# Kernel optimization log

Hardware: AMD Instinct MI355X
Metric: run time of the kernel (lower is better)

Reference implementation:

```python
import jax, jax.numpy as jnp
import numpy as np
from jax import lax

G0, G1 = 16, 16
UNITS = 256


def setup_inputs() -> dict:
    key = jax.random.key(0)
    ks = jax.random.split(key, 20)
    B, H, W, C = 64, 512, 512, 3
    U = UNITS
    flat = 12 * 12 * 3  # after two VALID 3x3 convs on 16x16x3
    inp = {
        'image': jax.random.normal(ks[0], (B, H, W, C), jnp.float32),
        'section': jax.random.uniform(ks[1], (B, 3), jnp.float32),
        'h0': jax.random.normal(ks[2], (B, U), jnp.float32) * 0.1,
        'c0': jax.random.normal(ks[3], (B, U), jnp.float32) * 0.1,
        'conv1_k': jax.random.normal(ks[4], (3, 3, C, 3), jnp.float32) * 0.2,
        'conv1_b': jnp.zeros((3,), jnp.float32),
        'conv2_k': jax.random.normal(ks[5], (3, 3, 3, 3), jnp.float32) * 0.2,
        'conv2_b': jnp.zeros((3,), jnp.float32),
        'dense_w': jax.random.normal(ks[6], (flat, U), jnp.float32) * (1.0 / np.sqrt(flat)),
        'dense_b': jnp.zeros((U,), jnp.float32),
        'lstm_k': jax.random.normal(ks[7], (U, 4 * U), jnp.float32) * (1.0 / np.sqrt(U)),
        'lstm_rk': jax.random.normal(ks[8], (U, 4 * U), jnp.float32) * (1.0 / np.sqrt(U)),
        'lstm_b': jnp.zeros((4 * U,), jnp.float32),
        'nsc_w1': jax.random.normal(ks[9], (U, U), jnp.float32) * (1.0 / np.sqrt(U)),
        'nsc_b1': jnp.zeros((U,), jnp.float32),
        'nsc_w2': jax.random.normal(ks[10], (U, 3), jnp.float32) * (1.0 / np.sqrt(U)),
        'nsc_b2': jnp.zeros((3,), jnp.float32),
    }
    return inp


def _interpolate(image, section):
    # image: (B,H,W,C); section: (B,3) = (x, y, scale); coords in [0,1],
    # mapped linearly onto grid indices with constant (clamp) extension,
    # matching tfp.math.batch_interp_regular_nd_grid over image axes 1,2.
    B, H, W, C = image.shape
    starts = section[:, :2]                       # (B,2)
    stops = section[:, :2] + section[:, 2:]       # (B,2) broadcast scale
    t0 = jnp.linspace(0.0, 1.0, G0)               # along grid_dim[0]
    alpha = jnp.linspace(0.0, 1.0, G1)            # along grid_dim[1]
    # p0[b,i,j]: coordinate mapped to image axis 1 (H)
    p0 = (starts[:, 0, None] + t0[None, :] * (stops[:, 0] - starts[:, 0])[:, None])[:, :, None]
    p0 = jnp.broadcast_to(p0, (B, G0, G1))
    # p1[b,i,j]: coordinate mapped to image axis 2 (W)
    p1 = (starts[:, 1, None] + alpha[None, :] * (stops[:, 1] - starts[:, 1])[:, None])[:, None, :]
    p1 = jnp.broadcast_to(p1, (B, G0, G1))
    fy = jnp.clip(p0 * (H - 1), 0.0, H - 1)
    fx = jnp.clip(p1 * (W - 1), 0.0, W - 1)
    y0 = jnp.floor(fy).astype(jnp.int32)
    x0 = jnp.floor(fx).astype(jnp.int32)
    y1 = jnp.minimum(y0 + 1, H - 1)
    x1 = jnp.minimum(x0 + 1, W - 1)
    wy = (fy - y0)[..., None]
    wx = (fx - x0)[..., None]
    b = jnp.arange(B)[:, None, None]
    v00 = image[b, y0, x0]
    v01 = image[b, y0, x1]
    v10 = image[b, y1, x0]
    v11 = image[b, y1, x1]
    top = v00 * (1 - wx) + v01 * wx
    bot = v10 * (1 - wx) + v11 * wx
    return top * (1 - wy) + bot * wy            # (B,G0,G1,C)


def _conv_relu(x, k, b):
    y = lax.conv_general_dilated(x, k, (1, 1), 'VALID',
                                 dimension_numbers=('NHWC', 'HWIO', 'NHWC'))
    return jax.nn.relu(y + b)


def reference(image, section, h0, c0, conv1_k, conv1_b, conv2_k, conv2_b,
              dense_w, dense_b, lstm_k, lstm_rk, lstm_b,
              nsc_w1, nsc_b1, nsc_w2, nsc_b2):
    sec = _interpolate(image, section)                 # (B,16,16,C)
    x = _conv_relu(sec, conv1_k, conv1_b)              # (B,14,14,3)
    x = _conv_relu(x, conv2_k, conv2_b)                # (B,12,12,3)
    x = x.reshape(x.shape[0], -1)                      # (B,432)
    x = jax.nn.relu(x @ dense_w + dense_b)             # (B,U)
    # Keras LSTMCell: gate order i, f, g(c), o
    z = x @ lstm_k + h0 @ lstm_rk + lstm_b
    i, f, g, o = jnp.split(z, 4, axis=-1)
    c_new = jax.nn.sigmoid(f) * c0 + jax.nn.sigmoid(i) * jnp.tanh(g)
    h_new = jax.nn.sigmoid(o) * jnp.tanh(c_new)
    nsc = jax.nn.relu(h_new @ nsc_w1 + nsc_b1)
    next_section = jax.nn.sigmoid(nsc @ nsc_w2 + nsc_b2)  # (B,3)
    return h_new, c_new, next_section
```

## Files before the change

kernel.cpp:

```cpp
#include <hip/hip_runtime.h>
#include <math.h>

#define BATCH 64
#define IMH 512
#define IMW 512
#define UNITS 256

__device__ __forceinline__ float sigmoidf_(float x) {
    return 1.0f / (1.0f + __expf(-x));
}
__device__ __forceinline__ float tanhf_(float x) {
    float e = __expf(2.0f * x);
    return 1.0f - 2.0f / (e + 1.0f);
}

#define WS_X   0
#define WS_Z   16384
#define WS_NSC (16384 + 65536)

__global__ __launch_bounds__(512) void k1_front(
    const float* __restrict__ image, const float* __restrict__ section,
    const float* __restrict__ k1, const float* __restrict__ b1,
    const float* __restrict__ k2, const float* __restrict__ b2,
    const float* __restrict__ dw, const float* __restrict__ db,
    float* __restrict__ ws)
{
    const int b   = blockIdx.x;
    const int tid = threadIdx.x;

    __shared__ float s_sec[16][16][3];
    __shared__ float s_c1[14][14][3];
    __shared__ float s_flat[432];
    __shared__ float s_part[2][256];
    __shared__ float s_k1[84];
    __shared__ float s_k2[84];

    if (tid < 81)       s_k1[tid]      = k1[tid];
    else if (tid < 84)  s_k1[tid]      = b1[tid - 81];
    else if (tid < 165) s_k2[tid - 84] = k2[tid - 84];
    else if (tid < 168) s_k2[tid - 84] = b2[tid - 165];

    if (tid < 256) {
        const float s0 = section[b * 3 + 0];
        const float s1 = section[b * 3 + 1];
        const float s2 = section[b * 3 + 2];
        const int i = tid >> 4, j = tid & 15;
        float p0 = s0 + (float)i * (1.0f / 15.0f) * s2;
        float p1 = s1 + (float)j * (1.0f / 15.0f) * s2;
        float fy = fminf(fmaxf(p0 * 511.0f, 0.0f), 511.0f);
        float fx = fminf(fmaxf(p1 * 511.0f, 0.0f), 511.0f);
        int y0 = (int)floorf(fy);
        int x0 = (int)floorf(fx);
        int y1 = min(y0 + 1, 511);
        int x1 = min(x0 + 1, 511);
        float wy = fy - (float)y0;
        float wx = fx - (float)x0;
        const float* base = image + (size_t)b * IMH * IMW * 3;
        const float* p00 = base + (y0 * IMW + x0) * 3;
        const float* p01 = base + (y0 * IMW + x1) * 3;
        const float* p10 = base + (y1 * IMW + x0) * 3;
        const float* p11 = base + (y1 * IMW + x1) * 3;
        #pragma unroll
        for (int c = 0; c < 3; ++c) {
            float top = p00[c] * (1.0f - wx) + p01[c] * wx;
            float bot = p10[c] * (1.0f - wx) + p11[c] * wx;
            s_sec[i][j][c] = top * (1.0f - wy) + bot * wy;
        }
    }
    __syncthreads();

    if (tid < 196) {
        const int i = tid / 14, j = tid % 14;
        float a0 = s_k1[81], a1 = s_k1[82], a2 = s_k1[83];
        #pragma unroll
        for (int di = 0; di < 3; ++di)
            #pragma unroll
            for (int dj = 0; dj < 3; ++dj)
                #pragma unroll
                for (int ci = 0; ci < 3; ++ci) {
                    float v = s_sec[i + di][j + dj][ci];
                    const int kb = ((di * 3 + dj) * 3 + ci) * 3;
                    a0 += v * s_k1[kb + 0];
                    a1 += v * s_k1[kb + 1];
                    a2 += v * s_k1[kb + 2];
                }
        s_c1[i][j][0] = fmaxf(a0, 0.0f);
        s_c1[i][j][1] = fmaxf(a1, 0.0f);
        s_c1[i][j][2] = fmaxf(a2, 0.0f);
    }
    __syncthreads();

    if (tid < 144) {
        const int i = tid / 12, j = tid % 12;
        float a0 = s_k2[81], a1 = s_k2[82], a2 = s_k2[83];
        #pragma unroll
        for (int di = 0; di < 3; ++di)
            #pragma unroll
            for (int dj = 0; dj < 3; ++dj)
                #pragma unroll
                for (int ci = 0; ci < 3; ++ci) {
                    float v = s_c1[i + di][j + dj][ci];
                    const int kb = ((di * 3 + dj) * 3 + ci) * 3;
                    a0 += v * s_k2[kb + 0];
                    a1 += v * s_k2[kb + 1];
                    a2 += v * s_k2[kb + 2];
                }
        const int fb = tid * 3;
        s_flat[fb + 0] = fmaxf(a0, 0.0f);
        s_flat[fb + 1] = fmaxf(a1, 0.0f);
        s_flat[fb + 2] = fmaxf(a2, 0.0f);
    }
    __syncthreads();

    {
        const int g = tid >> 8, col = tid & 255;
        const int k0 = g * 216;
        const float* fp = s_flat + k0;
        const float* wp = dw + k0 * 256 + col;
        float acc = 0.0f;
        #pragma unroll 8
        for (int k = 0; k < 216; ++k)
            acc += fp[k] * wp[k * 256];
        s_part[g][col] = acc;
    }
    __syncthreads();
    if (tid < 256)
        ws[WS_X + b * 256 + tid] =
            fmaxf(s_part[0][tid] + s_part[1][tid] + db[tid], 0.0f);
}

__global__ __launch_bounds__(256) void k2_lstm_gemm(
    const float* __restrict__ h0, const float* __restrict__ lk,
    const float* __restrict__ lrk, const float* __restrict__ lb,
    float* __restrict__ ws)
{
    const int bx   = blockIdx.x;
    const int ct   = bx & 15;
    const int bt   = bx >> 4;
    const int col0 = ct * 64;
    const int row0 = bt * 2;
    const int tid  = threadIdx.x;

    __shared__ float s_x2[2][256];
    __shared__ float s_h2[2][256];
    __shared__ float s_zp[2][128];

    for (int i = tid; i < 512; i += 256) {
        const int r = i >> 8, k = i & 255;
        s_x2[r][k] = ws[WS_X + (row0 + r) * 256 + k];
        s_h2[r][k] = h0[(row0 + r) * 256 + k];
    }
    __syncthreads();

    {
        const int c  = tid & 63;
        const int b2 = (tid >> 6) & 1;
        const int ks = tid >> 7;
        const int k0 = ks * 128;
        const float* lkp = lk  + (size_t)k0 * 1024 + col0 + c;
        const float* lrp = lrk + (size_t)k0 * 1024 + col0 + c;
        const float* xp = s_x2[b2] + k0;
        const float* hp = s_h2[b2] + k0;
        float acc = 0.0f;
        #pragma unroll 8
        for (int k = 0; k < 128; ++k)
            acc += xp[k] * lkp[k * 1024] + hp[k] * lrp[k * 1024];
        s_zp[ks][b2 * 64 + c] = acc;
    }
    __syncthreads();

    if (tid < 128) {
        const int c  = tid & 63;
        const int b2 = tid >> 6;
        ws[WS_Z + (row0 + b2) * 1024 + col0 + c] =
            s_zp[0][tid] + s_zp[1][tid] + lb[col0 + c];
    }
}

__global__ __launch_bounds__(256) void k4_cell_nsc1(
    const float* __restrict__ c0, const float* __restrict__ w1,
    const float* __restrict__ nb1, float* __restrict__ ws,
    float* __restrict__ out)
{
    const int bx   = blockIdx.x;
    const int ct   = bx & 3;
    const int bt   = bx >> 2;
    const int col0 = ct * 64;
    const int row0 = bt * 4;
    const int tid  = threadIdx.x;

    __shared__ float s_hn[4][256];

    {
        const int u = tid;
        #pragma unroll
        for (int b2 = 0; b2 < 4; ++b2) {
            const int row = row0 + b2;
            const float zi = ws[WS_Z + row * 1024 + u];
            const float zf = ws[WS_Z + row * 1024 + 256 + u];
            const float zg = ws[WS_Z + row * 1024 + 512 + u];
            const float zo = ws[WS_Z + row * 1024 + 768 + u];
            const float cprev = c0[row * 256 + u];
            const float cn = sigmoidf_(zf) * cprev + sigmoidf_(zi) * tanhf_(zg);
            const float hn = sigmoidf_(zo) * tanhf_(cn);
            s_hn[b2][u] = hn;
            if (ct == 0) {
                out[row * 256 + u] = hn;
                out[BATCH * UNITS + row * 256 + u] = cn;
            }
        }
    }
    __syncthreads();

    {
        const int c   = tid & 63;
        const int b2  = tid >> 6;
        const int col = col0 + c;
        const float* hp = s_hn[b2];
        const float* wp = w1 + col;
        float acc = nb1[col];
        #pragma unroll 8
        for (int k = 0; k < 256; ++k)
            acc += hp[k] * wp[k * 256];
        ws[WS_NSC + (row0 + b2) * 256 + col] = fmaxf(acc, 0.0f);
    }
}

__global__ __launch_bounds__(256) void k5_nsc2(
    const float* __restrict__ w2, const float* __restrict__ nb2,
    const float* __restrict__ ws, float* __restrict__ out)
{
    const int b   = blockIdx.x;
    const int tid = threadIdx.x;
    if (tid < 192) {
        const int j = tid >> 6;
        const int l = tid & 63;
        float p = 0.0f;
        #pragma unroll
        for (int k = l; k < 256; k += 64)
            p += ws[WS_NSC + b * 256 + k] * w2[k * 3 + j];
        #pragma unroll
        for (int off = 32; off > 0; off >>= 1)
            p += __shfl_down(p, off);
        if (l == 0)
            out[2 * BATCH * UNITS + b * 3 + j] = sigmoidf_(p + nb2[j]);
    }
}

extern "C" void kernel_launch(void* const* d_in, const int* in_sizes, int n_in,
                              void* d_out, int out_size, void* d_ws, size_t ws_size,
                              hipStream_t stream) {
    const float* image   = (const float*)d_in[0];
    const float* section = (const float*)d_in[1];
    const float* h0      = (const float*)d_in[2];
    const float* c0      = (const float*)d_in[3];
    const float* k1      = (const float*)d_in[4];
    const float* b1      = (const float*)d_in[5];
    const float* k2      = (const float*)d_in[6];
    const float* b2      = (const float*)d_in[7];
    const float* dw      = (const float*)d_in[8];
    const float* db      = (const float*)d_in[9];
    const float* lk      = (const float*)d_in[10];
    const float* lrk     = (const float*)d_in[11];
    const float* lb      = (const float*)d_in[12];
    const float* w1      = (const float*)d_in[13];
    const float* nb1     = (const float*)d_in[14];
    const float* w2      = (const float*)d_in[15];
    const float* nb2     = (const float*)d_in[16];
    float* out = (float*)d_out;
    float* ws  = (float*)d_ws;

    k1_front<<<64, 512, 0, stream>>>(image, section, k1, b1, k2, b2, dw, db, ws);
    k2_lstm_gemm<<<512, 256, 0, stream>>>(h0, lk, lrk, lb, ws);
    k4_cell_nsc1<<<64, 256, 0, stream>>>(c0, w1, nb1, ws, out);
    k5_nsc2<<<64, 256, 0, stream>>>(w2, nb2, ws, out);
}
```

Measured before the change: 304.5 us.

## Vectorize weight loads as float4 and retile GEMV kernels with deeper K-splits

The dense, LSTM and nsc1 matrix-vector stages now load weights as float4. Each thread accumulates four output columns over a shorter K slice, and the partial sums are reduced through shared memory. The LSTM GEMM handles four batch rows per block with half as many blocks, which reuses each weight load across more rows. nsc1 uses two rows per block with twice as many blocks. The aim is fewer, wider global loads and more memory-level parallelism, at the cost of extra shared-memory reduction work.

```diff
diff --git a/kernel.cpp b/kernel.cpp
--- a/kernel.cpp
+++ b/kernel.cpp
@@ -31,7 +31,7 @@
     __shared__ float s_sec[16][16][3];
     __shared__ float s_c1[14][14][3];
     __shared__ float s_flat[432];
-    __shared__ float s_part[2][256];
+    __shared__ float s_pf[2048];
     __shared__ float s_k1[84];
     __shared__ float s_k2[84];
 
@@ -113,20 +113,29 @@
     __syncthreads();
 
     {
-        const int g = tid >> 8, col = tid & 255;
-        const int k0 = g * 216;
+        const int ks = tid >> 6;
+        const int q  = tid & 63;
+        const int k0 = ks * 54;
+        const float4* wp = (const float4*)dw + (size_t)k0 * 64 + q;
         const float* fp = s_flat + k0;
-        const float* wp = dw + k0 * 256 + col;
-        float acc = 0.0f;
-        #pragma unroll 8
-        for (int k = 0; k < 216; ++k)
-            acc += fp[k] * wp[k * 256];
-        s_part[g][col] = acc;
-    }
-    __syncthreads();
-    if (tid < 256)
-        ws[WS_X + b * 256 + tid] =
-            fmaxf(s_part[0][tid] + s_part[1][tid] + db[tid], 0.0f);
+        float4 acc = {0.f, 0.f, 0.f, 0.f};
+        #pragma unroll 18
+        for (int k = 0; k < 54; ++k) {
+            const float4 w = wp[k * 64];
+            const float v = fp[k];
+            acc.x += v * w.x; acc.y += v * w.y; acc.z += v * w.z; acc.w += v * w.w;
+        }
+        ((float4*)s_pf)[ks * 64 + q] = acc;
+    }
+    __syncthreads();
+    if (tid < 256) {
+        const int q2 = tid >> 2, comp = tid & 3;
+        float a = db[tid];
+        #pragma unroll
+        for (int ks2 = 0; ks2 < 8; ++ks2)
+            a += s_pf[(ks2 * 64 + q2) * 4 + comp];
+        ws[WS_X + b * 256 + tid] = fmaxf(a, 0.0f);
+    }
 }
 
 __global__ __launch_bounds__(256) void k2_lstm_gemm(
@@ -134,67 +143,82 @@
     const float* __restrict__ lrk, const float* __restrict__ lb,
     float* __restrict__ ws)
 {
-    const int bx   = blockIdx.x;
-    const int ct   = bx & 15;
-    const int bt   = bx >> 4;
-    const int col0 = ct * 64;
-    const int row0 = bt * 2;
-    const int tid  = threadIdx.x;
-
-    __shared__ float s_x2[2][256];
-    __shared__ float s_h2[2][256];
-    __shared__ float s_zp[2][128];
-
-    for (int i = tid; i < 512; i += 256) {
+    const int bx    = blockIdx.x;
+    const int ct    = bx & 15;
+    const int bt    = bx >> 4;
+    const int col0  = ct * 64;
+    const int colq0 = ct * 16;
+    const int row0  = bt * 4;
+    const int tid   = threadIdx.x;
+
+    __shared__ float s_x4[4][256];
+    __shared__ float s_h4[4][256];
+    __shared__ float s_zpf[1024];
+
+    for (int i = tid; i < 1024; i += 256) {
         const int r = i >> 8, k = i & 255;
-        s_x2[r][k] = ws[WS_X + (row0 + r) * 256 + k];
-        s_h2[r][k] = h0[(row0 + r) * 256 + k];
-    }
-    __syncthreads();
-
-    {
-        const int c  = tid & 63;
-        const int b2 = (tid >> 6) & 1;
-        const int ks = tid >> 7;
-        const int k0 = ks * 128;
-        const float* lkp = lk  + (size_t)k0 * 1024 + col0 + c;
-        const float* lrp = lrk + (size_t)k0 * 1024 + col0 + c;
-        const float* xp = s_x2[b2] + k0;
-        const float* hp = s_h2[b2] + k0;
-        float acc = 0.0f;
-        #pragma unroll 8
-        for (int k = 0; k < 128; ++k)
-            acc += xp[k] * lkp[k * 1024] + hp[k] * lrp[k * 1024];
-        s_zp[ks][b2 * 64 + c] = acc;
-    }
-    __syncthreads();
-
-    if (tid < 128) {
-        const int c  = tid & 63;
-        const int b2 = tid >> 6;
-        ws[WS_Z + (row0 + b2) * 1024 + col0 + c] =
-            s_zp[0][tid] + s_zp[1][tid] + lb[col0 + c];
-    }
-}
-
-__global__ __launch_bounds__(256) void k4_cell_nsc1(
+        s_x4[r][k] = ws[WS_X + (row0 + r) * 256 + k];
+        s_h4[r][k] = h0[(row0 + r) * 256 + k];
+    }
+    __syncthreads();
+
+    {
+        const int q  = tid & 15;
+        const int bb = (tid >> 4) & 3;
+        const int ks = tid >> 6;
+        const int k0 = ks * 64;
+        const float4* lkp = (const float4*)lk  + (size_t)k0 * 256 + colq0 + q;
+        const float4* lrp = (const float4*)lrk + (size_t)k0 * 256 + colq0 + q;
+        const float* xp = s_x4[bb] + k0;
+        const float* hp = s_h4[bb] + k0;
+        float4 acc = {0.f, 0.f, 0.f, 0.f};
+        #pragma unroll 16
+        for (int k = 0; k < 64; ++k) {
+            const float4 a = lkp[k * 256];
+            const float4 r = lrp[k * 256];
+            const float xv = xp[k];
+            const float hv = hp[k];
+            acc.x += xv * a.x + hv * r.x;
+            acc.y += xv * a.y + hv * r.y;
+            acc.z += xv * a.z + hv * r.z;
+            acc.w += xv * a.w + hv * r.w;
+        }
+        ((float4*)s_zpf)[(ks * 4 + bb) * 16 + q] = acc;
+    }
+    __syncthreads();
+
+    {
+        const int c   = tid & 63;
+        const int bb2 = tid >> 6;
+        const int q2 = c >> 2, comp = c & 3;
+        float z = lb[col0 + c];
+        #pragma unroll
+        for (int ks2 = 0; ks2 < 4; ++ks2)
+            z += s_zpf[((ks2 * 4 + bb2) * 16 + q2) * 4 + comp];
+        ws[WS_Z + (row0 + bb2) * 1024 + col0 + c] = z;
+    }
+}
+
+__global__ __launch_bounds__(256) void k3_cell_nsc1(
     const float* __restrict__ c0, const float* __restrict__ w1,
     const float* __restrict__ nb1, float* __restrict__ ws,
     float* __restrict__ out)
 {
-    const int bx   = blockIdx.x;
-    const int ct   = bx & 3;
-    const int bt   = bx >> 2;
-    const int col0 = ct * 64;
-    const int row0 = bt * 4;
-    const int tid  = threadIdx.x;
-
-    __shared__ float s_hn[4][256];
+    const int bx    = blockIdx.x;
+    const int ct    = bx & 3;
+    const int bt    = bx >> 2;
+    const int col0  = ct * 64;
+    const int colq0 = ct * 16;
+    const int row0  = bt * 2;
+    const int tid   = threadIdx.x;
+
+    __shared__ float s_hn[2][256];
+    __shared__ float s_pf[1024];
 
     {
         const int u = tid;
         #pragma unroll
-        for (int b2 = 0; b2 < 4; ++b2) {
+        for (int b2 = 0; b2 < 2; ++b2) {
             const int row = row0 + b2;
             const float zi = ws[WS_Z + row * 1024 + u];
             const float zf = ws[WS_Z + row * 1024 + 256 + u];
@@ -213,38 +237,52 @@
     __syncthreads();
 
     {
+        const int q  = tid & 15;
+        const int bb = (tid >> 4) & 1;
+        const int ks = tid >> 5;
+        const int k0 = ks * 32;
+        const float4* wp = (const float4*)w1 + (size_t)k0 * 64 + colq0 + q;
+        const float* hp = s_hn[bb] + k0;
+        float4 acc = {0.f, 0.f, 0.f, 0.f};
+        #pragma unroll 16
+        for (int k = 0; k < 32; ++k) {
+            const float4 w = wp[k * 64];
+            const float v = hp[k];
+            acc.x += v * w.x; acc.y += v * w.y; acc.z += v * w.z; acc.w += v * w.w;
+        }
+        ((float4*)s_pf)[(ks * 2 + bb) * 16 + q] = acc;
+    }
+    __syncthreads();
+
+    if (tid < 128) {
         const int c   = tid & 63;
-        const int b2  = tid >> 6;
-        const int col = col0 + c;
-        const float* hp = s_hn[b2];
-        const float* wp = w1 + col;
-        float acc = nb1[col];
-        #pragma unroll 8
-        for (int k = 0; k < 256; ++k)
-            acc += hp[k] * wp[k * 256];
-        ws[WS_NSC + (row0 + b2) * 256 + col] = fmaxf(acc, 0.0f);
-    }
-}
-
-__global__ __launch_bounds__(256) void k5_nsc2(
+        const int bb2 = tid >> 6;
+        const int q2 = c >> 2, comp = c & 3;
+        float a = nb1[col0 + c];
+        #pragma unroll
+        for (int ks2 = 0; ks2 < 8; ++ks2)
+            a += s_pf[((ks2 * 2 + bb2) * 16 + q2) * 4 + comp];
+        ws[WS_NSC + (row0 + bb2) * 256 + col0 + c] = fmaxf(a, 0.0f);
+    }
+}
+
+__global__ __launch_bounds__(192) void k4_nsc2(
     const float* __restrict__ w2, const float* __restrict__ nb2,
     const float* __restrict__ ws, float* __restrict__ out)
 {
     const int b   = blockIdx.x;
     const int tid = threadIdx.x;
-    if (tid < 192) {
-        const int j = tid >> 6;
-        const int l = tid & 63;
-        float p = 0.0f;
-        #pragma unroll
-        for (int k = l; k < 256; k += 64)
-            p += ws[WS_NSC + b * 256 + k] * w2[k * 3 + j];
-        #pragma unroll
-        for (int off = 32; off > 0; off >>= 1)
-            p += __shfl_down(p, off);
-        if (l == 0)
-            out[2 * BATCH * UNITS + b * 3 + j] = sigmoidf_(p + nb2[j]);
-    }
+    const int j = tid >> 6;
+    const int l = tid & 63;
+    float p = 0.0f;
+    #pragma unroll
+    for (int k = l; k < 256; k += 64)
+        p += ws[WS_NSC + b * 256 + k] * w2[k * 3 + j];
+    #pragma unroll
+    for (int off = 32; off > 0; off >>= 1)
+        p += __shfl_down(p, off);
+    if (l == 0)
+        out[2 * BATCH * UNITS + b * 3 + j] = sigmoidf_(p + nb2[j]);
 }
 
 extern "C" void kernel_launch(void* const* d_in, const int* in_sizes, int n_in,
@@ -271,7 +309,7 @@
     float* ws  = (float*)d_ws;
 
     k1_front<<<64, 512, 0, stream>>>(image, section, k1, b1, k2, b2, dw, db, ws);
-    k2_lstm_gemm<<<512, 256, 0, stream>>>(h0, lk, lrk, lb, ws);
-    k4_cell_nsc1<<<64, 256, 0, stream>>>(c0, w1, nb1, ws, out);
-    k5_nsc2<<<64, 256, 0, stream>>>(w2, nb2, ws, out);
-}
+    k2_lstm_gemm<<<256, 256, 0, stream>>>(h0, lk, lrk, lb, ws);
+    k3_cell_nsc1<<<128, 256, 0, stream>>>(c0, w1, nb1, ws, out);
+    k4_nsc2<<<64, 192, 0, stream>>>(w2, nb2, ws, out);
+}
```

Result: no change. 302.6 us (-0.6%).
